# Kernel tuning notes

Measured on AMD Instinct MI355X. Metric: run time of the kernel, lower is better.

Reference implementation:

```python
import jax, jax.numpy as jnp
import numpy as np

B, C_IN, T = 16, 1, 10240
C = 256                # conv_dim_out == config.model.conv_channels
KERNEL, STRIDE, PAD = 10, 5, 0
K_STEPS = 12           # config.model.predict_steps
NEG = 10               # config.train.neg_samples
EPS = 1e-5
L_OUT = (T + 2 * PAD - KERNEL) // STRIDE + 1   # 2047


def setup_inputs() -> dict:
    key = jax.random.key(0)
    ks = jax.random.split(key, 5)
    return {
        "x": jax.random.normal(ks[0], (B, C_IN, T), jnp.float32),
        "conv_w": jax.random.normal(ks[1], (C, C_IN, KERNEL), jnp.float32) * 0.1,
        "conv_b": jnp.zeros((C,), jnp.float32),
        "bn_gamma": jnp.ones((C,), jnp.float32),
        "bn_beta": jnp.zeros((C,), jnp.float32),
        "tr_w": jax.random.normal(ks[2], (K_STEPS, C, C), jnp.float32) / np.sqrt(C).astype(np.float32),
        "tr_b": jnp.zeros((K_STEPS, C), jnp.float32),
        "perm": jax.random.permutation(ks[3], L_OUT),  # randperm over the time axis
    }


def reference(x, conv_w, conv_b, bn_gamma, bn_beta, tr_w, tr_b, perm):
    # ---- encoder: Conv1d -> ReLU -> BatchNorm1d (training-mode batch stats) ----
    h = jax.lax.conv_general_dilated(
        x, conv_w, window_strides=(STRIDE,), padding=[(PAD, PAD)],
        dimension_numbers=("NCH", "OIH", "NCH"))
    h = jax.nn.relu(h + conv_b[None, :, None])            # (B, C, L)
    mu = h.mean(axis=(0, 2), keepdims=True)
    var = h.var(axis=(0, 2), keepdims=True)               # biased, as torch BN
    h = (h - mu) * jax.lax.rsqrt(var + EPS)
    h = h * bn_gamma[None, :, None] + bn_beta[None, :, None]
    z = h.transpose(0, 2, 1)                              # (B, L, C)

    # ---- negatives: batch-roll by 1, random permutation of the time axis; detached ----
    z_negative = jax.lax.stop_gradient(jnp.roll(z, 1, axis=0)[:, perm, :])

    L = z.shape[1]
    # z_neg_full[b, i] == roll(z_neg, i, axis=0)[b] == z_neg[(b - i) % B]
    roll_idx = (jnp.arange(B)[:, None] - jnp.arange(NEG)[None, :]) % B  # (B, NEG)

    losses = []
    for k in range(1, K_STEPS + 1):
        l_len = L - k
        z_pos = z[:, k:, :]                               # (B, l, C)
        z_neg = z_negative[:, k:, :]                      # (B, l, C)
        z_neg_full = z_neg[roll_idx]                      # (B, NEG, l, C)
        W, bb = tr_w[k - 1], tr_b[k - 1]
        est_pos = (z_pos @ W + bb)[:, None]               # (B, 1, l, C)
        est_neg = z_neg_full @ W + bb                     # (B, NEG, l, C)
        estimated = jnp.concatenate([est_pos, est_neg], axis=1)        # (B, S, l, C)
        z_full = jnp.concatenate([z_pos[:, None], z_neg_full], axis=1)  # (B, S, l, C)
        f = jnp.einsum("bslc,bslc->bsl", estimated, z_full)
        # faithful to torch: flatten (b, s, l) row-major then view as (b*l, S)
        f_k = f.reshape(B * l_len, NEG + 1)
        logp = jax.nn.log_softmax(f_k, axis=1)
        losses.append(-logp.sum() / ((l_len - k) * B))

    # torch forward returns z.permute(0, 2, 1); losses returned too for baseline use
    return z.transpose(0, 2, 1), jnp.stack(losses)
```

## Files before the change

### kernel.cpp

```cpp
#include <hip/hip_runtime.h>
#include <hip/hip_bf16.h>
#include <math.h>

constexpr int B_ = 16;
constexpr int T_ = 10240;
constexpr int C_ = 256;
constexpr int KW = 10;
constexpr int L_ = 2047;
constexpr int N_ = B_ * L_;
constexpr int KSTEPS = 12;
constexpr float EPS_ = 1e-5f;
constexpr int QSTR = 32768;

typedef short bf16x8 __attribute__((ext_vector_type(8)));
typedef float f32x4  __attribute__((ext_vector_type(4)));

__global__ __launch_bounds__(256) void stats_wt_kernel(
    const float* __restrict__ x, const float* __restrict__ cw, const float* __restrict__ cb,
    float* __restrict__ ssum, float* __restrict__ ssq,
    const float* __restrict__ tw, __hip_bfloat16* __restrict__ Wt)
{
    __shared__ float smem[64 * 65];
    const int bid = blockIdx.x;
    if (bid < 256) {
        const int b  = bid & 15;
        const int l0 = (bid >> 4) * 128;
        const int cnt = min(128, L_ - l0);
        const int c = threadIdx.x;
        float* xs = smem;
        const float* xb = x + (size_t)b * T_;
        for (int i = threadIdx.x; i < cnt * 5 + 5; i += 256) xs[i] = xb[l0 * 5 + i];
        float w[KW];
#pragma unroll
        for (int j = 0; j < KW; ++j) w[j] = cw[c * KW + j];
        const float bias = cb[c];
        __syncthreads();
        float s = 0.f, s2 = 0.f;
        for (int dl = 0; dl < cnt; ++dl) {
            float v = bias;
#pragma unroll
            for (int j = 0; j < KW; ++j) v = fmaf(xs[dl * 5 + j], w[j], v);
            v = fmaxf(v, 0.f);
            s += v;
            s2 = fmaf(v, v, s2);
        }
        atomicAdd(&ssum[c], s);
        atomicAdd(&ssq[c], s2);
    } else {
        const int idx = bid - 256;
        const int k  = idx >> 4;
        const int c0 = ((idx & 15) >> 2) * 64, j0 = (idx & 3) * 64;
        float (*tile)[65] = (float(*)[65])smem;
        for (int i = threadIdx.x; i < 64 * 64; i += 256) {
            int c = i >> 6, j = i & 63;
            tile[c][j] = tw[((size_t)k * C_ + (c0 + c)) * C_ + j0 + j];
        }
        __syncthreads();
        for (int i = threadIdx.x; i < 64 * 64; i += 256) {
            int j = i >> 6, c = i & 63;
            Wt[((size_t)k * C_ + (j0 + j)) * C_ + c0 + c] = __float2bfloat16(tile[c][j]);
        }
    }
}

__global__ void bn_finalize_kernel(const float* __restrict__ ssum, const float* __restrict__ ssq,
                                   const float* __restrict__ gamma, const float* __restrict__ beta,
                                   float* __restrict__ scale, float* __restrict__ shift)
{
    int c = threadIdx.x;
    const float inv_n = 1.0f / (float)N_;
    float mu  = ssum[c] * inv_n;
    float var = ssq[c] * inv_n - mu * mu;
    float sc  = gamma[c] * rsqrtf(var + EPS_);
    scale[c] = sc;
    shift[c] = beta[c] - mu * sc;
}

__global__ __launch_bounds__(256) void conv_norm_kernel(
    const float* __restrict__ x, const float* __restrict__ cw, const float* __restrict__ cb,
    const float* __restrict__ scale, const float* __restrict__ shift,
    __hip_bfloat16* __restrict__ Zb, float* __restrict__ out0)
{
    const int b  = blockIdx.y;
    const int l0 = blockIdx.x * 32;
    const int cnt = min(32, L_ - l0);
    const int c = threadIdx.x;
    __shared__ float xs[32 * 5 + 8];
    __shared__ float zt[32][257];
    const float* xb = x + (size_t)b * T_;
    for (int i = threadIdx.x; i < cnt * 5 + 5; i += 256) xs[i] = xb[l0 * 5 + i];
    float w[KW];
#pragma unroll
    for (int j = 0; j < KW; ++j) w[j] = cw[c * KW + j];
    const float bias = cb[c];
    const float sc = scale[c], sh = shift[c];
    __syncthreads();
    for (int dl = 0; dl < cnt; ++dl) {
        float v = bias;
#pragma unroll
        for (int j = 0; j < KW; ++j) v = fmaf(xs[dl * 5 + j], w[j], v);
        v = fmaxf(v, 0.f);
        float z = fmaf(v, sc, sh);
        Zb[((size_t)(b * L_ + l0 + dl)) * C_ + c] = __float2bfloat16(z);
        zt[dl][c] = z;
    }
    __syncthreads();
    const int lq  = threadIdx.x & 31;
    const int cr0 = threadIdx.x >> 5;
    if (lq < cnt) {
#pragma unroll
        for (int i = 0; i < 32; ++i) {
            int cr = cr0 * 32 + i;
            out0[((size_t)(b * C_ + cr)) * L_ + l0 + lq] = zt[lq][cr];
        }
    }
}

__global__ __launch_bounds__(256, 2) void qmfma_kernel(
    const __hip_bfloat16* __restrict__ Zb, const __hip_bfloat16* __restrict__ Wt,
    const float* __restrict__ tb, float* __restrict__ qt)
{
    const int k   = blockIdx.y;
    const int grp = blockIdx.x;
    const __hip_bfloat16* __restrict__ Wk = Wt + (size_t)k * C_ * C_;

    __shared__ __hip_bfloat16 zs[2][32 * 256];
    __shared__ float qacc[4][256];

    const int tid  = threadIdx.x;
    const int lane = tid & 63, wave = tid >> 6;
    const int n16  = lane & 15, quad = lane >> 4;
    const int sw   = n16 & 7;

    bf16x8 wfrag[4][8];
    {
        const __hip_bfloat16* wb = Wk + ((size_t)(64 * wave + n16)) * C_ + quad * 8;
#pragma unroll
        for (int ct = 0; ct < 4; ++ct)
#pragma unroll
            for (int it = 0; it < 8; ++it)
                wfrag[ct][it] = *(const bf16x8*)(wb + ct * 16 * C_ + it * 32);
    }
    float4 bias4[4];
#pragma unroll
    for (int ct = 0; ct < 4; ++ct)
        bias4[ct] = *(const float4*)(tb + k * C_ + 64 * wave + ct * 16 + quad * 4);

    const int row0 = grp * 8 * 32;
    float4 greg[4];

#pragma unroll
    for (int i = 0; i < 4; ++i) {
        int chunk = tid + i * 256;
        int r = chunk >> 5;
        int rg = row0 + r; if (rg > N_ - 1) rg = N_ - 1;
        greg[i] = *(const float4*)(Zb + (size_t)rg * C_ + (chunk & 31) * 8);
    }
#pragma unroll
    for (int i = 0; i < 4; ++i) {
        int chunk = tid + i * 256;
        int r = chunk >> 5, j = chunk & 31;
        *(float4*)((__hip_bfloat16*)zs[0] + r * 256 + (j ^ (r & 7)) * 8) = greg[i];
    }
    __syncthreads();

    for (int t = 0; t < 8; ++t) {
        const int p = t & 1;

        if (t < 7) {
            int r0 = row0 + (t + 1) * 32;
#pragma unroll
            for (int i = 0; i < 4; ++i) {
                int chunk = tid + i * 256;
                int r = chunk >> 5;
                int rg = r0 + r; if (rg > N_ - 1) rg = N_ - 1;
                greg[i] = *(const float4*)(Zb + (size_t)rg * C_ + (chunk & 31) * 8);
            }
        }

        f32x4 acc[2][4];
#pragma unroll
        for (int rt = 0; rt < 2; ++rt)
#pragma unroll
            for (int ct = 0; ct < 4; ++ct) acc[rt][ct] = f32x4{0.f, 0.f, 0.f, 0.f};

        const __hip_bfloat16* zsp = (const __hip_bfloat16*)zs[p];
#pragma unroll
        for (int it = 0; it < 8; ++it) {
            const int js = (it * 4 + quad) ^ sw;
            bf16x8 zf0 = *(const bf16x8*)(zsp + n16 * 256 + js * 8);
            bf16x8 zf1 = *(const bf16x8*)(zsp + (n16 + 16) * 256 + js * 8);
#pragma unroll
            for (int ct = 0; ct < 4; ++ct) {
                acc[0][ct] = __builtin_amdgcn_mfma_f32_16x16x32_bf16(
                    wfrag[ct][it], zf0, acc[0][ct], 0, 0, 0);
                acc[1][ct] = __builtin_amdgcn_mfma_f32_16x16x32_bf16(
                    wfrag[ct][it], zf1, acc[1][ct], 0, 0, 0);
            }
        }

#pragma unroll
        for (int rt = 0; rt < 2; ++rt) {
            const int row = rt * 16 + n16;
            float s = 0.f;
#pragma unroll
            for (int ct = 0; ct < 4; ++ct) {
                const int j  = 8 * wave + 2 * ct + (quad >> 1);
                const char* zp = (const char*)zsp + row * 512 + ((j ^ sw) << 4) + (quad & 1) * 8;
                uint2 zz = *(const uint2*)zp;
                float z0 = __uint_as_float(zz.x << 16);
                float z1 = __uint_as_float(zz.x & 0xffff0000u);
                float z2 = __uint_as_float(zz.y << 16);
                float z3 = __uint_as_float(zz.y & 0xffff0000u);
                s = fmaf(acc[rt][ct][0] + bias4[ct].x, z0, s);
                s = fmaf(acc[rt][ct][1] + bias4[ct].y, z1, s);
                s = fmaf(acc[rt][ct][2] + bias4[ct].z, z2, s);
                s = fmaf(acc[rt][ct][3] + bias4[ct].w, z3, s);
            }
            s += __shfl_xor(s, 16);
            s += __shfl_xor(s, 32);
            if (lane < 16) qacc[wave][t * 32 + row] = s;
        }

        if (t < 7) {
#pragma unroll
            for (int i = 0; i < 4; ++i) {
                int chunk = tid + i * 256;
                int r = chunk >> 5, j = chunk & 31;
                *(float4*)((__hip_bfloat16*)zs[1 - p] + r * 256 + (j ^ (r & 7)) * 8) = greg[i];
            }
        }
        __syncthreads();
    }

    {
        int r  = tid;
        int rg = row0 + r;
        if (rg < N_) {
            float qv = qacc[0][r] + qacc[1][r] + qacc[2][r] + qacc[3][r];
            int b = rg / L_;
            int l = rg - b * L_;
            qt[(size_t)k * QSTR + (l << 4) + b] = qv;
        }
    }
}

__global__ __launch_bounds__(256) void loss_kernel(
    const float* __restrict__ qt, const int* __restrict__ perm, float* __restrict__ lacc)
{
    const int k = blockIdx.y + 1;
    const float* qk = qt + (size_t)(k - 1) * QSTR;
    const int nval = B_ * (L_ - k);
    const int idx = blockIdx.x * 256 + threadIdx.x;

    float contrib = 0.f;
    if (idx < nval) {
        int b = idx & 15;
        int l = k + (idx >> 4);
        float f0 = qk[(l << 4) | b];
        int pl = perm[l];
        const float* qn = qk + ((size_t)pl << 4);
        float f[10];
#pragma unroll
        for (int n = 0; n < 10; ++n) f[n] = qn[(b + 15 - n) & 15];
        float m = f0;
#pragma unroll
        for (int i = 0; i < 10; ++i) m = fmaxf(m, f[i]);
        float se = expf(f0 - m), fs = f0;
#pragma unroll
        for (int i = 0; i < 10; ++i) { se += expf(f[i] - m); fs += f[i]; }
        contrib = 11.f * (m + logf(se)) - fs;
    }

    __shared__ float red[4];
#pragma unroll
    for (int off = 32; off > 0; off >>= 1) contrib += __shfl_down(contrib, off);
    const int lane = threadIdx.x & 63;
    const int wave = threadIdx.x >> 6;
    if (lane == 0) red[wave] = contrib;
    __syncthreads();
    if (threadIdx.x == 0) atomicAdd(&lacc[k - 1], red[0] + red[1] + red[2] + red[3]);
}

__global__ void finalize_loss_kernel(const float* __restrict__ lacc, float* __restrict__ out1)
{
    int k = threadIdx.x;
    if (k < KSTEPS) {
        float div = (float)((L_ - 2 * (k + 1)) * B_);
        out1[k] = lacc[k] / div;
    }
}

extern "C" void kernel_launch(void* const* d_in, const int* in_sizes, int n_in,
                              void* d_out, int out_size, void* d_ws, size_t ws_size,
                              hipStream_t stream)
{
    const float* x     = (const float*)d_in[0];
    const float* cw    = (const float*)d_in[1];
    const float* cb    = (const float*)d_in[2];
    const float* gamma = (const float*)d_in[3];
    const float* beta  = (const float*)d_in[4];
    const float* tw    = (const float*)d_in[5];
    const float* tb    = (const float*)d_in[6];
    const int*   perm  = (const int*)d_in[7];

    float* out0 = (float*)d_out;
    float* out1 = out0 + (size_t)B_ * C_ * L_;

    char* ws = (char*)d_ws;
    __hip_bfloat16* Zb = (__hip_bfloat16*)ws;   ws += (size_t)N_ * C_ * 2;
    __hip_bfloat16* Wt = (__hip_bfloat16*)ws;   ws += (size_t)KSTEPS * C_ * C_ * 2;
    float* qt    = (float*)ws;                  ws += (size_t)KSTEPS * QSTR * 4;
    float* ssum  = (float*)ws;                  ws += C_ * 4;
    float* ssq   = (float*)ws;                  ws += C_ * 4;
    float* lacc  = (float*)ws;                  ws += 64 * 4;
    float* scale = (float*)ws;                  ws += C_ * 4;
    float* shift = (float*)ws;                  ws += C_ * 4;

    hipMemsetAsync(ssum, 0, (C_ + C_ + 64) * sizeof(float), stream);

    stats_wt_kernel<<<448, 256, 0, stream>>>(x, cw, cb, ssum, ssq, tw, Wt);
    bn_finalize_kernel<<<1, 256, 0, stream>>>(ssum, ssq, gamma, beta, scale, shift);

    dim3 gcv(64, 16);
    conv_norm_kernel<<<gcv, 256, 0, stream>>>(x, cw, cb, scale, shift, Zb, out0);

    dim3 gq(128, KSTEPS);
    qmfma_kernel<<<gq, 256, 0, stream>>>(Zb, Wt, tb, qt);

    dim3 gl(128, KSTEPS);
    loss_kernel<<<gl, 256, 0, stream>>>(qt, perm, lacc);
    finalize_loss_kernel<<<1, 64, 0, stream>>>(lacc, out1);
}
```

Measured before the change: 192.1 us.

## Rewrite q GEMM with 32x32 MFMA, async LDS loads, split-K waves, fused BN finalize

The q kernel now uses 512-thread blocks with 32x32x16 bf16 MFMAs and splits the channel reduction across two wave halves. It stages Z tiles into LDS with global_load_lds and raw barriers, and accumulates partial dot products into a zeroed qt buffer with atomics. The bias term is computed once in an extra grid row for all steps instead of per step. The BN finalize kernel is folded into conv_norm, removing a launch but adding a larger memset and atomic traffic.

```diff
diff --git a/kernel.cpp b/kernel.cpp
--- a/kernel.cpp
+++ b/kernel.cpp
@@ -14,6 +14,7 @@
 
 typedef short bf16x8 __attribute__((ext_vector_type(8)));
 typedef float f32x4  __attribute__((ext_vector_type(4)));
+typedef float f32x16 __attribute__((ext_vector_type(16)));
 
 __global__ __launch_bounds__(256) void stats_wt_kernel(
     const float* __restrict__ x, const float* __restrict__ cw, const float* __restrict__ cb,
@@ -63,22 +64,10 @@
     }
 }
 
-__global__ void bn_finalize_kernel(const float* __restrict__ ssum, const float* __restrict__ ssq,
-                                   const float* __restrict__ gamma, const float* __restrict__ beta,
-                                   float* __restrict__ scale, float* __restrict__ shift)
-{
-    int c = threadIdx.x;
-    const float inv_n = 1.0f / (float)N_;
-    float mu  = ssum[c] * inv_n;
-    float var = ssq[c] * inv_n - mu * mu;
-    float sc  = gamma[c] * rsqrtf(var + EPS_);
-    scale[c] = sc;
-    shift[c] = beta[c] - mu * sc;
-}
-
 __global__ __launch_bounds__(256) void conv_norm_kernel(
     const float* __restrict__ x, const float* __restrict__ cw, const float* __restrict__ cb,
-    const float* __restrict__ scale, const float* __restrict__ shift,
+    const float* __restrict__ ssum, const float* __restrict__ ssq,
+    const float* __restrict__ gamma, const float* __restrict__ beta,
     __hip_bfloat16* __restrict__ Zb, float* __restrict__ out0)
 {
     const int b  = blockIdx.y;
@@ -93,7 +82,11 @@
 #pragma unroll
     for (int j = 0; j < KW; ++j) w[j] = cw[c * KW + j];
     const float bias = cb[c];
-    const float sc = scale[c], sh = shift[c];
+    const float inv_n = 1.0f / (float)N_;
+    const float mu  = ssum[c] * inv_n;
+    const float var = ssq[c] * inv_n - mu * mu;
+    const float sc  = gamma[c] * rsqrtf(var + EPS_);
+    const float sh  = beta[c] - mu * sc;
     __syncthreads();
     for (int dl = 0; dl < cnt; ++dl) {
         float v = bias;
@@ -116,133 +109,168 @@
     }
 }
 
-__global__ __launch_bounds__(256, 2) void qmfma_kernel(
+__global__ __launch_bounds__(512, 4) void qmfma_kernel(
     const __hip_bfloat16* __restrict__ Zb, const __hip_bfloat16* __restrict__ Wt,
     const float* __restrict__ tb, float* __restrict__ qt)
 {
     const int k   = blockIdx.y;
     const int grp = blockIdx.x;
-    const __hip_bfloat16* __restrict__ Wk = Wt + (size_t)k * C_ * C_;
 
     __shared__ __hip_bfloat16 zs[2][32 * 256];
-    __shared__ float qacc[4][256];
+    __shared__ float qaccU[8 * 384];
 
     const int tid  = threadIdx.x;
     const int lane = tid & 63, wave = tid >> 6;
-    const int n16  = lane & 15, quad = lane >> 4;
-    const int sw   = n16 & 7;
-
-    bf16x8 wfrag[4][8];
-    {
-        const __hip_bfloat16* wb = Wk + ((size_t)(64 * wave + n16)) * C_ + quad * 8;
-#pragma unroll
-        for (int ct = 0; ct < 4; ++ct)
-#pragma unroll
-            for (int it = 0; it < 8; ++it)
-                wfrag[ct][it] = *(const bf16x8*)(wb + ct * 16 * C_ + it * 32);
-    }
-    float4 bias4[4];
-#pragma unroll
-    for (int ct = 0; ct < 4; ++ct)
-        bias4[ct] = *(const float4*)(tb + k * C_ + 64 * wave + ct * 16 + quad * 4);
-
-    const int row0 = grp * 8 * 32;
-    float4 greg[4];
-
-#pragma unroll
-    for (int i = 0; i < 4; ++i) {
-        int chunk = tid + i * 256;
-        int r = chunk >> 5;
-        int rg = row0 + r; if (rg > N_ - 1) rg = N_ - 1;
-        greg[i] = *(const float4*)(Zb + (size_t)rg * C_ + (chunk & 31) * 8);
-    }
-#pragma unroll
-    for (int i = 0; i < 4; ++i) {
-        int chunk = tid + i * 256;
-        int r = chunk >> 5, j = chunk & 31;
-        *(float4*)((__hip_bfloat16*)zs[0] + r * 256 + (j ^ (r & 7)) * 8) = greg[i];
-    }
-    __syncthreads();
-
-    for (int t = 0; t < 8; ++t) {
-        const int p = t & 1;
-
-        if (t < 7) {
-            int r0 = row0 + (t + 1) * 32;
-#pragma unroll
-            for (int i = 0; i < 4; ++i) {
-                int chunk = tid + i * 256;
-                int r = chunk >> 5;
-                int rg = r0 + r; if (rg > N_ - 1) rg = N_ - 1;
-                greg[i] = *(const float4*)(Zb + (size_t)rg * C_ + (chunk & 31) * 8);
-            }
-        }
-
-        f32x4 acc[2][4];
-#pragma unroll
-        for (int rt = 0; rt < 2; ++rt)
-#pragma unroll
-            for (int ct = 0; ct < 4; ++ct) acc[rt][ct] = f32x4{0.f, 0.f, 0.f, 0.f};
-
-        const __hip_bfloat16* zsp = (const __hip_bfloat16*)zs[p];
-#pragma unroll
-        for (int it = 0; it < 8; ++it) {
-            const int js = (it * 4 + quad) ^ sw;
-            bf16x8 zf0 = *(const bf16x8*)(zsp + n16 * 256 + js * 8);
-            bf16x8 zf1 = *(const bf16x8*)(zsp + (n16 + 16) * 256 + js * 8);
-#pragma unroll
-            for (int ct = 0; ct < 4; ++ct) {
-                acc[0][ct] = __builtin_amdgcn_mfma_f32_16x16x32_bf16(
-                    wfrag[ct][it], zf0, acc[0][ct], 0, 0, 0);
-                acc[1][ct] = __builtin_amdgcn_mfma_f32_16x16x32_bf16(
-                    wfrag[ct][it], zf1, acc[1][ct], 0, 0, 0);
-            }
-        }
-
-#pragma unroll
-        for (int rt = 0; rt < 2; ++rt) {
-            const int row = rt * 16 + n16;
+    const int n31  = lane & 31, h = lane >> 5;
+    const int sw   = n31 & 7;
+    const int row0 = grp * 256;
+
+    const int c0 = wave * 128 + lane;
+    const int c1 = c0 + 64;
+    const int r0_ = c0 >> 5; const int j0_ = (c0 & 31) ^ (r0_ & 7);
+    const int r1_ = c1 >> 5; const int j1_ = (c1 & 31) ^ (r1_ & 7);
+
+#define STAGE(buf, t) do {                                                                 \
+    int rg0 = row0 + (t) * 32 + r0_; if (rg0 > N_ - 1) rg0 = N_ - 1;                       \
+    int rg1 = row0 + (t) * 32 + r1_; if (rg1 > N_ - 1) rg1 = N_ - 1;                       \
+    __builtin_amdgcn_global_load_lds(                                                      \
+        (const __attribute__((address_space(1))) void*)(Zb + (size_t)rg0 * C_ + j0_ * 8),  \
+        (__attribute__((address_space(3))) void*)(&zs[buf][wave * 1024]), 16, 0, 0);       \
+    __builtin_amdgcn_global_load_lds(                                                      \
+        (const __attribute__((address_space(1))) void*)(Zb + (size_t)rg1 * C_ + j1_ * 8),  \
+        (__attribute__((address_space(3))) void*)(&zs[buf][wave * 1024 + 512]), 16, 0, 0); \
+} while (0)
+
+    if (k < KSTEPS) {
+        const int cg = wave & 3, kh = wave >> 2;
+        bf16x8 wfrag[2][8];
+        {
+            const __hip_bfloat16* wb =
+                Wt + ((size_t)k * C_ + 64 * cg + n31) * C_ + 128 * kh + h * 8;
+#pragma unroll
+            for (int ct = 0; ct < 2; ++ct)
+#pragma unroll
+                for (int it = 0; it < 8; ++it)
+                    wfrag[ct][it] = *(const bf16x8*)(wb + (size_t)ct * 32 * C_ + it * 16);
+        }
+        STAGE(0, 0);
+        asm volatile("s_waitcnt vmcnt(0)" ::: "memory");
+        __builtin_amdgcn_s_barrier();
+
+        int p = 0;
+        for (int t = 0; t < 8; ++t, p ^= 1) {
+            if (t < 7) {
+                STAGE(p ^ 1, t + 1);
+                asm volatile("s_waitcnt vmcnt(2)" ::: "memory");
+            } else {
+                asm volatile("s_waitcnt vmcnt(0)" ::: "memory");
+            }
+            __builtin_amdgcn_s_barrier();
+
+            const __hip_bfloat16* zsp = zs[p];
+            f32x16 acc0, acc1;
+#pragma unroll
+            for (int i = 0; i < 16; ++i) { acc0[i] = 0.f; acc1[i] = 0.f; }
+#pragma unroll
+            for (int it = 0; it < 8; ++it) {
+                const int chunk = kh * 16 + it * 2 + h;
+                bf16x8 zf = *(const bf16x8*)(zsp + n31 * 256 + ((chunk ^ sw) * 8));
+                acc0 = __builtin_amdgcn_mfma_f32_32x32x16_bf16(wfrag[0][it], zf, acc0, 0, 0, 0);
+                acc1 = __builtin_amdgcn_mfma_f32_32x32x16_bf16(wfrag[1][it], zf, acc1, 0, 0, 0);
+            }
             float s = 0.f;
 #pragma unroll
-            for (int ct = 0; ct < 4; ++ct) {
-                const int j  = 8 * wave + 2 * ct + (quad >> 1);
-                const char* zp = (const char*)zsp + row * 512 + ((j ^ sw) << 4) + (quad & 1) * 8;
+            for (int ct = 0; ct < 2; ++ct) {
+#pragma unroll
+                for (int g2 = 0; g2 < 4; ++g2) {
+                    const int chunk = 8 * cg + 4 * ct + g2;
+                    const char* zp = (const char*)zsp + n31 * 512 + ((chunk ^ sw) << 4) + 8 * h;
+                    uint2 zz = *(const uint2*)zp;
+                    float z0 = __uint_as_float(zz.x << 16);
+                    float z1 = __uint_as_float(zz.x & 0xffff0000u);
+                    float z2 = __uint_as_float(zz.y << 16);
+                    float z3 = __uint_as_float(zz.y & 0xffff0000u);
+                    const f32x16& a = ct ? acc1 : acc0;
+                    s = fmaf(a[g2 * 4 + 0], z0, s);
+                    s = fmaf(a[g2 * 4 + 1], z1, s);
+                    s = fmaf(a[g2 * 4 + 2], z2, s);
+                    s = fmaf(a[g2 * 4 + 3], z3, s);
+                }
+            }
+            s += __shfl_xor(s, 32);
+            if (lane < 32) qaccU[wave * 256 + t * 32 + n31] = s;
+            asm volatile("s_waitcnt lgkmcnt(0)" ::: "memory");
+            __builtin_amdgcn_s_barrier();
+        }
+        if (tid < 256) {
+            int rg = row0 + tid;
+            if (rg < N_) {
+                float qv = 0.f;
+#pragma unroll
+                for (int w2 = 0; w2 < 8; ++w2) qv += qaccU[w2 * 256 + tid];
+                int b = rg / L_;
+                int l = rg - b * L_;
+                atomicAdd(&qt[(size_t)k * QSTR + (l << 4) + b], qv);
+            }
+        }
+    } else {
+        STAGE(0, 0);
+        asm volatile("s_waitcnt vmcnt(0)" ::: "memory");
+        __builtin_amdgcn_s_barrier();
+
+        int p = 0;
+        for (int t = 0; t < 8; ++t, p ^= 1) {
+            if (t < 7) {
+                STAGE(p ^ 1, t + 1);
+                asm volatile("s_waitcnt vmcnt(2)" ::: "memory");
+            } else {
+                asm volatile("s_waitcnt vmcnt(0)" ::: "memory");
+            }
+            __builtin_amdgcn_s_barrier();
+
+            const __hip_bfloat16* zsp = zs[p];
+            float zv[16];
+#pragma unroll
+            for (int g2 = 0; g2 < 4; ++g2) {
+                const int chunk = 4 * wave + g2;
+                const char* zp = (const char*)zsp + n31 * 512 + ((chunk ^ sw) << 4) + 8 * h;
                 uint2 zz = *(const uint2*)zp;
-                float z0 = __uint_as_float(zz.x << 16);
-                float z1 = __uint_as_float(zz.x & 0xffff0000u);
-                float z2 = __uint_as_float(zz.y << 16);
-                float z3 = __uint_as_float(zz.y & 0xffff0000u);
-                s = fmaf(acc[rt][ct][0] + bias4[ct].x, z0, s);
-                s = fmaf(acc[rt][ct][1] + bias4[ct].y, z1, s);
-                s = fmaf(acc[rt][ct][2] + bias4[ct].z, z2, s);
-                s = fmaf(acc[rt][ct][3] + bias4[ct].w, z3, s);
-            }
-            s += __shfl_xor(s, 16);
-            s += __shfl_xor(s, 32);
-            if (lane < 16) qacc[wave][t * 32 + row] = s;
-        }
-
-        if (t < 7) {
-#pragma unroll
-            for (int i = 0; i < 4; ++i) {
-                int chunk = tid + i * 256;
-                int r = chunk >> 5, j = chunk & 31;
-                *(float4*)((__hip_bfloat16*)zs[1 - p] + r * 256 + (j ^ (r & 7)) * 8) = greg[i];
-            }
-        }
-        __syncthreads();
-    }
-
-    {
-        int r  = tid;
-        int rg = row0 + r;
-        if (rg < N_) {
-            float qv = qacc[0][r] + qacc[1][r] + qacc[2][r] + qacc[3][r];
-            int b = rg / L_;
-            int l = rg - b * L_;
-            qt[(size_t)k * QSTR + (l << 4) + b] = qv;
-        }
-    }
+                zv[g2 * 4 + 0] = __uint_as_float(zz.x << 16);
+                zv[g2 * 4 + 1] = __uint_as_float(zz.x & 0xffff0000u);
+                zv[g2 * 4 + 2] = __uint_as_float(zz.y << 16);
+                zv[g2 * 4 + 3] = __uint_as_float(zz.y & 0xffff0000u);
+            }
+#pragma unroll
+            for (int kk = 0; kk < KSTEPS; ++kk) {
+                float sk = 0.f;
+#pragma unroll
+                for (int g2 = 0; g2 < 4; ++g2) {
+                    float4 b4 = *(const float4*)(tb + kk * C_ + 32 * wave + 8 * g2 + 4 * h);
+                    sk = fmaf(b4.x, zv[g2 * 4 + 0], sk);
+                    sk = fmaf(b4.y, zv[g2 * 4 + 1], sk);
+                    sk = fmaf(b4.z, zv[g2 * 4 + 2], sk);
+                    sk = fmaf(b4.w, zv[g2 * 4 + 3], sk);
+                }
+                sk += __shfl_xor(sk, 32);
+                if (lane < 32) qaccU[wave * 384 + kk * 32 + n31] = sk;
+            }
+            asm volatile("s_waitcnt lgkmcnt(0)" ::: "memory");
+            __builtin_amdgcn_s_barrier();
+            if (tid < 384) {
+                int kk = tid >> 5, row = tid & 31;
+                int rg = row0 + t * 32 + row;
+                if (rg < N_) {
+                    float qv = 0.f;
+#pragma unroll
+                    for (int w2 = 0; w2 < 8; ++w2) qv += qaccU[w2 * 384 + kk * 32 + row];
+                    int b = rg / L_;
+                    int l = rg - b * L_;
+                    atomicAdd(&qt[(size_t)kk * QSTR + (l << 4) + b], qv);
+                }
+            }
+        }
+    }
+#undef STAGE
 }
 
 __global__ __launch_bounds__(256) void loss_kernel(
@@ -308,25 +336,22 @@
     float* out1 = out0 + (size_t)B_ * C_ * L_;
 
     char* ws = (char*)d_ws;
+    float* qt   = (float*)ws;                   ws += (size_t)KSTEPS * QSTR * 4;
+    float* ssum = (float*)ws;                   ws += C_ * 4;
+    float* ssq  = (float*)ws;                   ws += C_ * 4;
+    float* lacc = (float*)ws;                   ws += 64 * 4;
     __hip_bfloat16* Zb = (__hip_bfloat16*)ws;   ws += (size_t)N_ * C_ * 2;
     __hip_bfloat16* Wt = (__hip_bfloat16*)ws;   ws += (size_t)KSTEPS * C_ * C_ * 2;
-    float* qt    = (float*)ws;                  ws += (size_t)KSTEPS * QSTR * 4;
-    float* ssum  = (float*)ws;                  ws += C_ * 4;
-    float* ssq   = (float*)ws;                  ws += C_ * 4;
-    float* lacc  = (float*)ws;                  ws += 64 * 4;
-    float* scale = (float*)ws;                  ws += C_ * 4;
-    float* shift = (float*)ws;                  ws += C_ * 4;
-
-    hipMemsetAsync(ssum, 0, (C_ + C_ + 64) * sizeof(float), stream);
+
+    hipMemsetAsync(qt, 0, (size_t)(KSTEPS * QSTR + C_ + C_ + 64) * sizeof(float), stream);
 
     stats_wt_kernel<<<448, 256, 0, stream>>>(x, cw, cb, ssum, ssq, tw, Wt);
-    bn_finalize_kernel<<<1, 256, 0, stream>>>(ssum, ssq, gamma, beta, scale, shift);
 
     dim3 gcv(64, 16);
-    conv_norm_kernel<<<gcv, 256, 0, stream>>>(x, cw, cb, scale, shift, Zb, out0);
-
-    dim3 gq(128, KSTEPS);
-    qmfma_kernel<<<gq, 256, 0, stream>>>(Zb, Wt, tb, qt);
+    conv_norm_kernel<<<gcv, 256, 0, stream>>>(x, cw, cb, ssum, ssq, gamma, beta, Zb, out0);
+
+    dim3 gq(128, KSTEPS + 1);
+    qmfma_kernel<<<gq, 512, 0, stream>>>(Zb, Wt, tb, qt);
 
     dim3 gl(128, KSTEPS);
     loss_kernel<<<gl, 256, 0, stream>>>(qt, perm, lacc);
```

New measurement: 259.0 us. 34.8% more time.

## Stage Z tiles via direct global-to-LDS loads with 4-deep pipeline; fold BN finalize

Applied to the files above, without the earlier changes.

The projection kernel now copies Z rows straight into shared memory with global_load_lds across four LDS buffers, two tiles ahead, replacing the register round-trip and double buffer. Explicit vmcnt waits and raw barriers stand in for __syncthreads, and MFMA priority is raised around the inner loop. The BN finalize kernel is removed and each conv block recomputes scale and shift itself, saving one launch. Costs are double the LDS per block, which may cut occupancy, and a risk that the hand-counted waits do not match the loads in flight.

```diff
diff --git a/kernel.cpp b/kernel.cpp
--- a/kernel.cpp
+++ b/kernel.cpp
@@ -63,22 +63,10 @@
     }
 }
 
-__global__ void bn_finalize_kernel(const float* __restrict__ ssum, const float* __restrict__ ssq,
-                                   const float* __restrict__ gamma, const float* __restrict__ beta,
-                                   float* __restrict__ scale, float* __restrict__ shift)
-{
-    int c = threadIdx.x;
-    const float inv_n = 1.0f / (float)N_;
-    float mu  = ssum[c] * inv_n;
-    float var = ssq[c] * inv_n - mu * mu;
-    float sc  = gamma[c] * rsqrtf(var + EPS_);
-    scale[c] = sc;
-    shift[c] = beta[c] - mu * sc;
-}
-
 __global__ __launch_bounds__(256) void conv_norm_kernel(
     const float* __restrict__ x, const float* __restrict__ cw, const float* __restrict__ cb,
-    const float* __restrict__ scale, const float* __restrict__ shift,
+    const float* __restrict__ ssum, const float* __restrict__ ssq,
+    const float* __restrict__ gamma, const float* __restrict__ beta,
     __hip_bfloat16* __restrict__ Zb, float* __restrict__ out0)
 {
     const int b  = blockIdx.y;
@@ -93,7 +81,11 @@
 #pragma unroll
     for (int j = 0; j < KW; ++j) w[j] = cw[c * KW + j];
     const float bias = cb[c];
-    const float sc = scale[c], sh = shift[c];
+    const float inv_n = 1.0f / (float)N_;
+    const float mu  = ssum[c] * inv_n;
+    const float var = ssq[c] * inv_n - mu * mu;
+    const float sc  = gamma[c] * rsqrtf(var + EPS_);
+    const float sh  = beta[c] - mu * sc;
     __syncthreads();
     for (int dl = 0; dl < cnt; ++dl) {
         float v = bias;
@@ -124,13 +116,14 @@
     const int grp = blockIdx.x;
     const __hip_bfloat16* __restrict__ Wk = Wt + (size_t)k * C_ * C_;
 
-    __shared__ __hip_bfloat16 zs[2][32 * 256];
+    __shared__ __hip_bfloat16 zs[4][32 * 256];
     __shared__ float qacc[4][256];
 
     const int tid  = threadIdx.x;
     const int lane = tid & 63, wave = tid >> 6;
     const int n16  = lane & 15, quad = lane >> 4;
     const int sw   = n16 & 7;
+    const int row0 = grp * 8 * 32;
 
     bf16x8 wfrag[4][8];
     {
@@ -146,37 +139,32 @@
     for (int ct = 0; ct < 4; ++ct)
         bias4[ct] = *(const float4*)(tb + k * C_ + 64 * wave + ct * 16 + quad * 4);
 
-    const int row0 = grp * 8 * 32;
-    float4 greg[4];
-
-#pragma unroll
-    for (int i = 0; i < 4; ++i) {
-        int chunk = tid + i * 256;
-        int r = chunk >> 5;
-        int rg = row0 + r; if (rg > N_ - 1) rg = N_ - 1;
-        greg[i] = *(const float4*)(Zb + (size_t)rg * C_ + (chunk & 31) * 8);
-    }
-#pragma unroll
-    for (int i = 0; i < 4; ++i) {
-        int chunk = tid + i * 256;
-        int r = chunk >> 5, j = chunk & 31;
-        *(float4*)((__hip_bfloat16*)zs[0] + r * 256 + (j ^ (r & 7)) * 8) = greg[i];
-    }
-    __syncthreads();
-
+#define STAGE(buf, t) do {                                                                  \
+    _Pragma("unroll")                                                                       \
+    for (int i_ = 0; i_ < 4; ++i_) {                                                        \
+        int rr = (wave * 4 + i_) * 2 + (lane >> 5);                                         \
+        int rg = row0 + (t) * 32 + rr; if (rg > N_ - 1) rg = N_ - 1;                        \
+        int jj = (lane & 31) ^ (rr & 7);                                                    \
+        __builtin_amdgcn_global_load_lds(                                                   \
+            (const __attribute__((address_space(1))) void*)(Zb + (size_t)rg * C_ + jj * 8), \
+            (__attribute__((address_space(3))) void*)(&zs[buf][(wave * 4 + i_) * 512]),     \
+            16, 0, 0);                                                                      \
+    }                                                                                       \
+} while (0)
+
+    STAGE(0, 0);
+    STAGE(1, 1);
+    asm volatile("s_waitcnt vmcnt(0)" ::: "memory");
+
+#pragma unroll
     for (int t = 0; t < 8; ++t) {
-        const int p = t & 1;
-
-        if (t < 7) {
-            int r0 = row0 + (t + 1) * 32;
-#pragma unroll
-            for (int i = 0; i < 4; ++i) {
-                int chunk = tid + i * 256;
-                int r = chunk >> 5;
-                int rg = r0 + r; if (rg > N_ - 1) rg = N_ - 1;
-                greg[i] = *(const float4*)(Zb + (size_t)rg * C_ + (chunk & 31) * 8);
-            }
-        }
+        if (t < 6) STAGE((t + 2) & 3, t + 2);
+        if (t >= 2 && t < 6)      { asm volatile("s_waitcnt vmcnt(8)" ::: "memory"); }
+        else if (t == 6)          { asm volatile("s_waitcnt vmcnt(4)" ::: "memory"); }
+        else if (t == 7)          { asm volatile("s_waitcnt vmcnt(0)" ::: "memory"); }
+        __builtin_amdgcn_s_barrier();
+
+        const __hip_bfloat16* zsp = (const __hip_bfloat16*)zs[t & 3];
 
         f32x4 acc[2][4];
 #pragma unroll
@@ -184,7 +172,7 @@
 #pragma unroll
             for (int ct = 0; ct < 4; ++ct) acc[rt][ct] = f32x4{0.f, 0.f, 0.f, 0.f};
 
-        const __hip_bfloat16* zsp = (const __hip_bfloat16*)zs[p];
+        __builtin_amdgcn_s_setprio(1);
 #pragma unroll
         for (int it = 0; it < 8; ++it) {
             const int js = (it * 4 + quad) ^ sw;
@@ -198,6 +186,7 @@
                     wfrag[ct][it], zf1, acc[1][ct], 0, 0, 0);
             }
         }
+        __builtin_amdgcn_s_setprio(0);
 
 #pragma unroll
         for (int rt = 0; rt < 2; ++rt) {
@@ -221,18 +210,10 @@
             s += __shfl_xor(s, 32);
             if (lane < 16) qacc[wave][t * 32 + row] = s;
         }
-
-        if (t < 7) {
-#pragma unroll
-            for (int i = 0; i < 4; ++i) {
-                int chunk = tid + i * 256;
-                int r = chunk >> 5, j = chunk & 31;
-                *(float4*)((__hip_bfloat16*)zs[1 - p] + r * 256 + (j ^ (r & 7)) * 8) = greg[i];
-            }
-        }
-        __syncthreads();
-    }
-
+    }
+#undef STAGE
+
+    __syncthreads();
     {
         int r  = tid;
         int rg = row0 + r;
@@ -314,16 +295,13 @@
     float* ssum  = (float*)ws;                  ws += C_ * 4;
     float* ssq   = (float*)ws;                  ws += C_ * 4;
     float* lacc  = (float*)ws;                  ws += 64 * 4;
-    float* scale = (float*)ws;                  ws += C_ * 4;
-    float* shift = (float*)ws;                  ws += C_ * 4;
 
     hipMemsetAsync(ssum, 0, (C_ + C_ + 64) * sizeof(float), stream);
 
     stats_wt_kernel<<<448, 256, 0, stream>>>(x, cw, cb, ssum, ssq, tw, Wt);
-    bn_finalize_kernel<<<1, 256, 0, stream>>>(ssum, ssq, gamma, beta, scale, shift);
 
     dim3 gcv(64, 16);
-    conv_norm_kernel<<<gcv, 256, 0, stream>>>(x, cw, cb, scale, shift, Zb, out0);
+    conv_norm_kernel<<<gcv, 256, 0, stream>>>(x, cw, cb, ssum, ssq, gamma, beta, Zb, out0);
 
     dim3 gq(128, KSTEPS);
     qmfma_kernel<<<gq, 256, 0, stream>>>(Zb, Wt, tb, qt);
```

New measurement: 190.3 us. No clear change (-0.9%).
